# Kernel tuning notes

Measured on AMD Instinct MI355X. Metric: run time of the kernel, lower is better.

Reference implementation:

```python
import jax, jax.numpy as jnp
import numpy as np

N_WORDS, MAX_LEN = 16384, 16
VOCAB, EMB, HID = 128, 64, 256


def setup_inputs() -> dict:
    key = jax.random.key(0)
    ks = jax.random.split(key, 11)
    s = 1.0 / np.sqrt(HID)  # torch LSTMCell default init scale
    u = lambda k, shape: jax.random.uniform(k, shape, jnp.float32, -s, s)
    return {
        "char_ids": jax.random.randint(ks[0], (N_WORDS, MAX_LEN), 0, VOCAB, dtype=jnp.int32),
        "lengths": jax.random.randint(ks[1], (N_WORDS,), 1, MAX_LEN + 1, dtype=jnp.int32),
        "emb": jax.random.normal(ks[2], (VOCAB, EMB), jnp.float32),
        "W_ih_f": u(ks[3], (4 * HID, EMB)),
        "W_hh_f": u(ks[4], (4 * HID, HID)),
        "b_ih_f": u(ks[5], (4 * HID,)),
        "b_hh_f": u(ks[6], (4 * HID,)),
        "W_ih_b": u(ks[7], (4 * HID, EMB)),
        "W_hh_b": u(ks[8], (4 * HID, HID)),
        "b_ih_b": u(ks[9], (4 * HID,)),
        "b_hh_b": u(ks[10], (4 * HID,)),
    }


def _run_lstm(xs, mask, W_ih, W_hh, b):
    # xs: [T, N, E]; mask: [T, N]; returns final masked hidden state [N, H]
    n = xs.shape[1]
    h0 = jnp.zeros((n, W_hh.shape[1]), xs.dtype)

    def step(carry, inp):
        h, c = carry
        x, m = inp
        gates = x @ W_ih.T + h @ W_hh.T + b  # [N, 4H], torch gate order i,f,g,o
        i, f, g, o = jnp.split(gates, 4, axis=-1)
        c2 = jax.nn.sigmoid(f) * c + jax.nn.sigmoid(i) * jnp.tanh(g)
        h2 = jax.nn.sigmoid(o) * jnp.tanh(c2)
        m = m[:, None]
        return (jnp.where(m, h2, h), jnp.where(m, c2, c)), None

    (h, _), _ = jax.lax.scan(step, (h0, h0), (xs, mask))
    return h


def reference(char_ids, lengths, emb, W_ih_f, W_hh_f, b_ih_f, b_hh_f,
              W_ih_b, W_hh_b, b_ih_b, b_hh_b):
    x = emb[char_ids]                                   # [N, T, E]
    t = jnp.arange(MAX_LEN)
    mask = t[None, :] < lengths[:, None]                # [N, T] valid chars
    xs = x.transpose(1, 0, 2)                           # [T, N, E]
    ms = mask.T                                         # [T, N]
    h_f = _run_lstm(xs, ms, W_ih_f, W_hh_f, b_ih_f + b_hh_f)
    # per-word reversed sequence: chars processed from last to first
    ridx = jnp.clip(lengths[:, None] - 1 - t[None, :], 0)  # [N, T]
    xr = jnp.take_along_axis(x, ridx[:, :, None], axis=1)  # [N, T, E]
    h_b = _run_lstm(xr.transpose(1, 0, 2), ms, W_ih_b, W_hh_b, b_ih_b + b_hh_b)
    return jnp.concatenate([h_f, h_b], axis=-1)         # [N, 2H]
```

## Files before the change

### kernel.cpp

```cpp
#include <hip/hip_runtime.h>

#define N_WORDS 16384
#define MAXL    16
#define VOCABSZ 128
#define EMBD    64
#define HID     256
#define GATES   1024
#define KTOT    320
#define AROW    328
#define M_TILE  64
#define NT      256

typedef __attribute__((ext_vector_type(8))) short bf16x8;
typedef __attribute__((ext_vector_type(4))) float f32x4;
typedef __attribute__((ext_vector_type(4))) int   i32x4;

#define OFF_WSW   0ul
#define OFF_EMB   1310720ul
#define OFF_BIAS  1327104ul
#define OFF_SORT  1335296ul

__device__ inline short tobf(float f) {
  unsigned u = __float_as_uint(f);
  unsigned r = (u + 0x7fffu + ((u >> 16) & 1u)) >> 16;
  return (short)r;
}
__device__ inline float aexp2(float x) { float r; asm("v_exp_f32 %0, %1" : "=v"(r) : "v"(x)); return r; }
__device__ inline float arcp(float x)  { float r; asm("v_rcp_f32 %0, %1" : "=v"(r) : "v"(x)); return r; }
__device__ inline float fsig(float x)   { return arcp(1.0f + aexp2(x * -1.4426950408889634f)); }
__device__ inline float ftanhf(float x) { return 1.0f - 2.0f * arcp(1.0f + aexp2(x * 2.8853900817779268f)); }

__global__ void prep_all(const float* __restrict__ Wihf, const float* __restrict__ Whhf,
                         const float* __restrict__ Wihb, const float* __restrict__ Whhb,
                         const float* __restrict__ emb,
                         const float* __restrict__ bihf, const float* __restrict__ bhhf,
                         const float* __restrict__ bihb, const float* __restrict__ bhhb,
                         const int* __restrict__ lengths,
                         short* __restrict__ wsw, short* __restrict__ embw,
                         float* __restrict__ biasg, int* __restrict__ sorted) {
  __shared__ int hist[16], base[16], cnt[16];
  int blk = blockIdx.x;
  if (blk < 320) {
    int id = blk * 256 + threadIdx.x;
    int d    = id / 40960;
    int r    = id % 40960;
    int R    = r / 640;
    int r2   = r % 640;
    int kk   = r2 / 64;
    int lane = r2 % 64;
    int m    = lane & 15;
    int unit = R * 4 + (m >> 2);
    int ty   = m & 3;
    int g    = ty * 256 + unit;
    int kb   = kk * 32 + (lane >> 4) * 8;
    const float* Wih = d ? Wihb : Wihf;
    const float* Whh = d ? Whhb : Whhf;
    bf16x8 v;
#pragma unroll
    for (int j = 0; j < 8; ++j) {
      int k = kb + j;
      float f = (k < HID) ? Whh[g * HID + k] : Wih[g * EMBD + (k - HID)];
      v[j] = tobf(f);
    }
    ((bf16x8*)wsw)[id] = v;
  } else if (blk < 360) {
    int id = (blk - 320) * 256 + threadIdx.x;
    if (id < VOCABSZ * EMBD) {
      embw[id] = tobf(emb[id]);
    } else {
      int r = id - VOCABSZ * EMBD;
      if (r < 2048) {
        int d = r >> 10, n = r & 1023;
        int g = (n & 3) * 256 + (n >> 2);
        biasg[r] = d ? (bihb[g] + bhhb[g]) : (bihf[g] + bhhf[g]);
      }
    }
  } else {
    int tid = threadIdx.x;
    if (tid < 16) { hist[tid] = 0; cnt[tid] = 0; }
    __syncthreads();
    for (int i = tid; i < N_WORDS; i += 256)
      atomicAdd(&hist[lengths[i] - 1], 1);
    __syncthreads();
    if (tid == 0) {
      int s = 0;
      for (int b = 0; b < 16; ++b) { base[b] = s; s += hist[b]; }
    }
    __syncthreads();
    for (int i = tid; i < N_WORDS; i += 256) {
      int b = lengths[i] - 1;
      int p = base[b] + atomicAdd(&cnt[b], 1);
      sorted[p] = i;
    }
  }
}

__global__ __launch_bounds__(512, 1) void lstm_main(
    const int* __restrict__ char_ids, const int* __restrict__ lengths,
    const short* __restrict__ wsw, const short* __restrict__ embw,
    const float* __restrict__ biasg, const int* __restrict__ sorted,
    float* __restrict__ out) {
  __shared__ __align__(16) short A[M_TILE * AROW];
  __shared__ __align__(16) int   charl[M_TILE * 16];
  __shared__ __align__(16) float biasl[GATES];
  __shared__ __align__(16) f32x4 c4[8 * 8 * 64];
  __shared__ int lenl[M_TILE];
  __shared__ int swl[M_TILE];

  const int tid  = threadIdx.x;
  const int lane = tid & 63;
  const int wv   = tid >> 6;
  const int quad = lane >> 4;
  const int colc = lane & 15;
  const int pb   = blockIdx.x;
  const int dir  = pb & 1;
  const int qb   = pb >> 1;
  const int tile = (qb & 1) ? (255 - (qb >> 1)) : (qb >> 1);

  if (tid < M_TILE) {
    int sw = sorted[tile * M_TILE + tid];
    swl[tid]  = sw;
    lenl[tid] = lengths[sw];
  }
  if (tid < 256) ((f32x4*)biasl)[tid] = ((const f32x4*)(biasg + dir * GATES))[tid];
  for (int i = tid; i < M_TILE * AROW / 2; i += 512) ((int*)A)[i] = 0;
  for (int i = tid; i < 8 * 8 * 64; i += 512) c4[i] = (f32x4){0.f, 0.f, 0.f, 0.f};
  __syncthreads();

  if (tid < 256) {
    int w = tid >> 2, ch = tid & 3;
    ((i32x4*)charl)[tid] = ((const i32x4*)(char_ids + swl[w] * 16))[ch];
  }
  int Lmax = lenl[lane];
  for (int o = 32; o; o >>= 1) { int v = __shfl_xor(Lmax, o, 64); Lmax = Lmax > v ? Lmax : v; }
  __syncthreads();

  auto gather_x = [&](int tt) {
    int wl = wv * 8 + (lane >> 3);
    int part = lane & 7;
    int lw = lenl[wl];
    int pos = (dir == 0) ? tt : (lw - 1 - tt);
    pos = pos < 0 ? 0 : (pos > 15 ? 15 : pos);
    int cid = charl[wl * 16 + pos];
    bf16x8 e = *(const bf16x8*)(embw + cid * EMBD + part * 8);
    *(bf16x8*)(A + wl * AROW + HID + part * 8) = e;
  };
  gather_x(0);

  int lenw[4], hadrb[4], oadr[4];
#pragma unroll
  for (int ct = 0; ct < 4; ++ct) {
    int wl = ct * 16 + colc;
    lenw[ct]  = lenl[wl];
    hadrb[ct] = wl * AROW + 32 * wv + quad;
    oadr[ct]  = swl[wl] * 512 + dir * 256 + 32 * wv + quad;
  }
  const short* wp = wsw + ((size_t)dir * 64 + wv * 8) * 10 * 64 * 8 + lane * 8;
  f32x4* cptr = c4 + wv * (8 * 64) + lane;

  __syncthreads();

  bf16x8 wA[10], wB[10];
#pragma unroll
  for (int kk = 0; kk < 10; ++kk) wA[kk] = *(const bf16x8*)(wp + kk * 512);

#pragma unroll 1
  for (int t = 0; t < Lmax; ++t) {
    bf16x8 hx[4][10];
#pragma unroll
    for (int ct = 0; ct < 4; ++ct)
#pragma unroll
      for (int kk = 0; kk < 10; ++kk)
        hx[ct][kk] = *(const bf16x8*)(A + (ct * 16 + colc) * AROW + kk * 32 + quad * 8);

    __syncthreads();

    auto wtile = [&](int rt, bf16x8(&wc)[10], bf16x8(&wn)[10], int pre) {
#pragma unroll
      for (int kk = 0; kk < 10; ++kk) wn[kk] = *(const bf16x8*)(wp + (pre * 10 + kk) * 512);
      f32x4 co4 = cptr[rt * 64];
      f32x4 bias4 = *(const f32x4*)(biasl + 128 * wv + 16 * rt + 4 * quad);
      f32x4 acc[4];
#pragma unroll
      for (int ct = 0; ct < 4; ++ct) acc[ct] = bias4;
#pragma unroll
      for (int kk = 0; kk < 10; ++kk)
#pragma unroll
        for (int ct = 0; ct < 4; ++ct)
          acc[ct] = __builtin_amdgcn_mfma_f32_16x16x32_bf16(wc[kk], hx[ct][kk], acc[ct], 0, 0, 0);

      f32x4 cnew;
#pragma unroll
      for (int ct = 0; ct < 4; ++ct) {
        float ig = fsig(acc[ct][0]);
        float fg = fsig(acc[ct][1]);
        float gg = ftanhf(acc[ct][2]);
        float og = fsig(acc[ct][3]);
        float co_v = co4[ct];
        float c2 = fg * co_v + ig * gg;
        float h2 = og * ftanhf(c2);
        bool act = t < lenw[ct];
        cnew[ct] = act ? c2 : co_v;
        if (act) A[hadrb[ct] + 4 * rt] = tobf(h2);
        if (t == lenw[ct] - 1) out[oadr[ct] + 4 * rt] = h2;
      }
      cptr[rt * 64] = cnew;
    };

#pragma unroll 1
    for (int rt2 = 0; rt2 < 8; rt2 += 2) {
      wtile(rt2,     wA, wB, rt2 + 1);
      wtile(rt2 + 1, wB, wA, (rt2 + 2) & 7);
    }

    gather_x(t + 1);
    __syncthreads();
  }
}

extern "C" void kernel_launch(void* const* d_in, const int* in_sizes, int n_in,
                              void* d_out, int out_size, void* d_ws, size_t ws_size,
                              hipStream_t stream) {
  const int*   char_ids = (const int*)d_in[0];
  const int*   lengths  = (const int*)d_in[1];
  const float* emb      = (const float*)d_in[2];
  const float* Wihf     = (const float*)d_in[3];
  const float* Whhf     = (const float*)d_in[4];
  const float* bihf     = (const float*)d_in[5];
  const float* bhhf     = (const float*)d_in[6];
  const float* Wihb     = (const float*)d_in[7];
  const float* Whhb     = (const float*)d_in[8];
  const float* bihb     = (const float*)d_in[9];
  const float* bhhb     = (const float*)d_in[10];

  char* ws = (char*)d_ws;
  short* wsw   = (short*)(ws + OFF_WSW);
  short* embw  = (short*)(ws + OFF_EMB);
  float* biasg = (float*)(ws + OFF_BIAS);
  int*   sortd = (int*)(ws + OFF_SORT);

  prep_all<<<361, 256, 0, stream>>>(Wihf, Whhf, Wihb, Whhb, emb,
                                    bihf, bhhf, bihb, bhhb, lengths,
                                    wsw, embw, biasg, sortd);
  lstm_main<<<512, 512, 0, stream>>>(char_ids, lengths, wsw, embw, biasg, sortd,
                                     (float*)d_out);
}
```

Baseline: 405.2 us.

## Double-buffer LSTM hidden-state tile to drop one barrier per timestep

Splits the shared A tile into two ping-pong buffers so each step reads h from one buffer and writes the new h into the other. This removes the mid-step __syncthreads, leaving a single raw s_barrier per step. The embedding gather is issued before the last two gate tiles so its latency overlaps MFMA work. The length masking on c and h is dropped, so words keep updating after their last character; this relies on outputs being written at t==len-1 and the sorted-by-length tiles. Costs an extra 42KB of LDS.

```diff
diff --git a/kernel.cpp b/kernel.cpp
--- a/kernel.cpp
+++ b/kernel.cpp
@@ -100,7 +100,8 @@
     const short* __restrict__ wsw, const short* __restrict__ embw,
     const float* __restrict__ biasg, const int* __restrict__ sorted,
     float* __restrict__ out) {
-  __shared__ __align__(16) short A[M_TILE * AROW];
+  __shared__ __align__(16) short A0[M_TILE * AROW];
+  __shared__ __align__(16) short A1[M_TILE * AROW];
   __shared__ __align__(16) int   charl[M_TILE * 16];
   __shared__ __align__(16) float biasl[GATES];
   __shared__ __align__(16) f32x4 c4[8 * 8 * 64];
@@ -123,7 +124,7 @@
     lenl[tid] = lengths[sw];
   }
   if (tid < 256) ((f32x4*)biasl)[tid] = ((const f32x4*)(biasg + dir * GATES))[tid];
-  for (int i = tid; i < M_TILE * AROW / 2; i += 512) ((int*)A)[i] = 0;
+  for (int i = tid; i < M_TILE * AROW / 2; i += 512) ((int*)A0)[i] = 0;
   for (int i = tid; i < 8 * 8 * 64; i += 512) c4[i] = (f32x4){0.f, 0.f, 0.f, 0.f};
   __syncthreads();
 
@@ -135,17 +136,19 @@
   for (int o = 32; o; o >>= 1) { int v = __shfl_xor(Lmax, o, 64); Lmax = Lmax > v ? Lmax : v; }
   __syncthreads();
 
-  auto gather_x = [&](int tt) {
-    int wl = wv * 8 + (lane >> 3);
-    int part = lane & 7;
-    int lw = lenl[wl];
+  const int xwl   = wv * 8 + (lane >> 3);
+  const int xpart = lane & 7;
+  auto x_load = [&](int tt) -> bf16x8 {
+    int lw = lenl[xwl];
     int pos = (dir == 0) ? tt : (lw - 1 - tt);
     pos = pos < 0 ? 0 : (pos > 15 ? 15 : pos);
-    int cid = charl[wl * 16 + pos];
-    bf16x8 e = *(const bf16x8*)(embw + cid * EMBD + part * 8);
-    *(bf16x8*)(A + wl * AROW + HID + part * 8) = e;
+    int cid = charl[xwl * 16 + pos];
+    return *(const bf16x8*)(embw + cid * EMBD + xpart * 8);
   };
-  gather_x(0);
+  auto x_store = [&](short* An, bf16x8 e) {
+    *(bf16x8*)(An + xwl * AROW + HID + xpart * 8) = e;
+  };
+  x_store(A0, x_load(0));
 
   int lenw[4], hadrb[4], oadr[4];
 #pragma unroll
@@ -164,6 +167,9 @@
 #pragma unroll
   for (int kk = 0; kk < 10; ++kk) wA[kk] = *(const bf16x8*)(wp + kk * 512);
 
+  short* Ac = A0;
+  short* An = A1;
+
 #pragma unroll 1
   for (int t = 0; t < Lmax; ++t) {
     bf16x8 hx[4][10];
@@ -171,9 +177,7 @@
     for (int ct = 0; ct < 4; ++ct)
 #pragma unroll
       for (int kk = 0; kk < 10; ++kk)
-        hx[ct][kk] = *(const bf16x8*)(A + (ct * 16 + colc) * AROW + kk * 32 + quad * 8);
-
-    __syncthreads();
+        hx[ct][kk] = *(const bf16x8*)(Ac + (ct * 16 + colc) * AROW + kk * 32 + quad * 8);
 
     auto wtile = [&](int rt, bf16x8(&wc)[10], bf16x8(&wn)[10], int pre) {
 #pragma unroll
@@ -196,25 +200,27 @@
         float fg = fsig(acc[ct][1]);
         float gg = ftanhf(acc[ct][2]);
         float og = fsig(acc[ct][3]);
-        float co_v = co4[ct];
-        float c2 = fg * co_v + ig * gg;
+        float c2 = fg * co4[ct] + ig * gg;
         float h2 = og * ftanhf(c2);
-        bool act = t < lenw[ct];
-        cnew[ct] = act ? c2 : co_v;
-        if (act) A[hadrb[ct] + 4 * rt] = tobf(h2);
+        cnew[ct] = c2;
+        An[hadrb[ct] + 4 * rt] = tobf(h2);
         if (t == lenw[ct] - 1) out[oadr[ct] + 4 * rt] = h2;
       }
       cptr[rt * 64] = cnew;
     };
 
 #pragma unroll 1
-    for (int rt2 = 0; rt2 < 8; rt2 += 2) {
+    for (int rt2 = 0; rt2 < 6; rt2 += 2) {
       wtile(rt2,     wA, wB, rt2 + 1);
-      wtile(rt2 + 1, wB, wA, (rt2 + 2) & 7);
-    }
-
-    gather_x(t + 1);
-    __syncthreads();
+      wtile(rt2 + 1, wB, wA, rt2 + 2);
+    }
+    bf16x8 e = x_load(t + 1);
+    wtile(6, wA, wB, 7);
+    wtile(7, wB, wA, 0);
+    x_store(An, e);
+
+    asm volatile("s_waitcnt lgkmcnt(0)\n\ts_barrier" ::: "memory");
+    short* tmp = Ac; Ac = An; An = tmp;
   }
 }
 
```

Result: slower. 573.9 us (+41.6%).

## Halve word tile to 32, run two 256-thread blocks per CU, split MFMA chains

Applied to the files above, without the earlier changes.

Each LSTM block now handles 32 length-sorted words with 4 waves, and each wave covers 16 gate row-tiles instead of 8. There are 1024 blocks at two per CU, so one block's barrier-bound recurrence can overlap another's. Each MFMA accumulation is split into two independent chains for more instruction-level parallelism. Masking of h/c writes after a word ends is dropped, since outputs are captured at the last valid step. In exchange, the weight stream is re-read by twice as many blocks, which raises L2/global weight traffic per word.

```diff
diff --git a/kernel.cpp b/kernel.cpp
--- a/kernel.cpp
+++ b/kernel.cpp
@@ -8,11 +8,12 @@
 #define GATES   1024
 #define KTOT    320
 #define AROW    328
-#define M_TILE  64
-#define NT      256
+#define M_TILE  32
+#define NT      512
 
 typedef __attribute__((ext_vector_type(8))) short bf16x8;
 typedef __attribute__((ext_vector_type(4))) float f32x4;
+typedef __attribute__((ext_vector_type(2))) float f32x2;
 typedef __attribute__((ext_vector_type(4))) int   i32x4;
 
 #define OFF_WSW   0ul
@@ -95,7 +96,7 @@
   }
 }
 
-__global__ __launch_bounds__(512, 1) void lstm_main(
+__global__ __launch_bounds__(256, 2) void lstm_main(
     const int* __restrict__ char_ids, const int* __restrict__ lengths,
     const short* __restrict__ wsw, const short* __restrict__ embw,
     const float* __restrict__ biasg, const int* __restrict__ sorted,
@@ -103,7 +104,7 @@
   __shared__ __align__(16) short A[M_TILE * AROW];
   __shared__ __align__(16) int   charl[M_TILE * 16];
   __shared__ __align__(16) float biasl[GATES];
-  __shared__ __align__(16) f32x4 c4[8 * 8 * 64];
+  __shared__ __align__(8)  f32x2 c4[4 * 16 * 64];
   __shared__ int lenl[M_TILE];
   __shared__ int swl[M_TILE];
 
@@ -115,23 +116,23 @@
   const int pb   = blockIdx.x;
   const int dir  = pb & 1;
   const int qb   = pb >> 1;
-  const int tile = (qb & 1) ? (255 - (qb >> 1)) : (qb >> 1);
+  const int tile = (qb & 1) ? (511 - (qb >> 1)) : (qb >> 1);
 
   if (tid < M_TILE) {
     int sw = sorted[tile * M_TILE + tid];
     swl[tid]  = sw;
     lenl[tid] = lengths[sw];
   }
-  if (tid < 256) ((f32x4*)biasl)[tid] = ((const f32x4*)(biasg + dir * GATES))[tid];
-  for (int i = tid; i < M_TILE * AROW / 2; i += 512) ((int*)A)[i] = 0;
-  for (int i = tid; i < 8 * 8 * 64; i += 512) c4[i] = (f32x4){0.f, 0.f, 0.f, 0.f};
+  ((f32x4*)biasl)[tid] = ((const f32x4*)(biasg + dir * GATES))[tid];
+  for (int i = tid; i < M_TILE * AROW / 2; i += 256) ((int*)A)[i] = 0;
+  for (int i = tid; i < 4 * 16 * 64; i += 256) c4[i] = (f32x2){0.f, 0.f};
   __syncthreads();
 
-  if (tid < 256) {
+  if (tid < 128) {
     int w = tid >> 2, ch = tid & 3;
     ((i32x4*)charl)[tid] = ((const i32x4*)(char_ids + swl[w] * 16))[ch];
   }
-  int Lmax = lenl[lane];
+  int Lmax = lenl[lane & 31];
   for (int o = 32; o; o >>= 1) { int v = __shfl_xor(Lmax, o, 64); Lmax = Lmax > v ? Lmax : v; }
   __syncthreads();
 
@@ -147,16 +148,16 @@
   };
   gather_x(0);
 
-  int lenw[4], hadrb[4], oadr[4];
-#pragma unroll
-  for (int ct = 0; ct < 4; ++ct) {
+  int lenw[2], hadrb[2], oadr[2];
+#pragma unroll
+  for (int ct = 0; ct < 2; ++ct) {
     int wl = ct * 16 + colc;
     lenw[ct]  = lenl[wl];
-    hadrb[ct] = wl * AROW + 32 * wv + quad;
-    oadr[ct]  = swl[wl] * 512 + dir * 256 + 32 * wv + quad;
-  }
-  const short* wp = wsw + ((size_t)dir * 64 + wv * 8) * 10 * 64 * 8 + lane * 8;
-  f32x4* cptr = c4 + wv * (8 * 64) + lane;
+    hadrb[ct] = wl * AROW + 64 * wv + quad;
+    oadr[ct]  = swl[wl] * 512 + dir * 256 + 64 * wv + quad;
+  }
+  const short* wp = wsw + ((size_t)dir * 64 + wv * 16) * 10 * 64 * 8 + lane * 8;
+  f32x2* cptr = c4 + wv * (16 * 64) + lane;
 
   __syncthreads();
 
@@ -166,9 +167,9 @@
 
 #pragma unroll 1
   for (int t = 0; t < Lmax; ++t) {
-    bf16x8 hx[4][10];
-#pragma unroll
-    for (int ct = 0; ct < 4; ++ct)
+    bf16x8 hx[2][10];
+#pragma unroll
+    for (int ct = 0; ct < 2; ++ct)
 #pragma unroll
       for (int kk = 0; kk < 10; ++kk)
         hx[ct][kk] = *(const bf16x8*)(A + (ct * 16 + colc) * AROW + kk * 32 + quad * 8);
@@ -178,39 +179,40 @@
     auto wtile = [&](int rt, bf16x8(&wc)[10], bf16x8(&wn)[10], int pre) {
 #pragma unroll
       for (int kk = 0; kk < 10; ++kk) wn[kk] = *(const bf16x8*)(wp + (pre * 10 + kk) * 512);
-      f32x4 co4 = cptr[rt * 64];
-      f32x4 bias4 = *(const f32x4*)(biasl + 128 * wv + 16 * rt + 4 * quad);
-      f32x4 acc[4];
-#pragma unroll
-      for (int ct = 0; ct < 4; ++ct) acc[ct] = bias4;
-#pragma unroll
-      for (int kk = 0; kk < 10; ++kk)
-#pragma unroll
-        for (int ct = 0; ct < 4; ++ct)
-          acc[ct] = __builtin_amdgcn_mfma_f32_16x16x32_bf16(wc[kk], hx[ct][kk], acc[ct], 0, 0, 0);
-
-      f32x4 cnew;
-#pragma unroll
-      for (int ct = 0; ct < 4; ++ct) {
-        float ig = fsig(acc[ct][0]);
-        float fg = fsig(acc[ct][1]);
-        float gg = ftanhf(acc[ct][2]);
-        float og = fsig(acc[ct][3]);
-        float co_v = co4[ct];
-        float c2 = fg * co_v + ig * gg;
+      f32x2 co2 = cptr[rt * 64];
+      f32x4 bias4 = *(const f32x4*)(biasl + 256 * wv + 16 * rt + 4 * quad);
+      f32x4 aL[2], aH[2];
+#pragma unroll
+      for (int ct = 0; ct < 2; ++ct) { aL[ct] = bias4; aH[ct] = (f32x4){0.f,0.f,0.f,0.f}; }
+#pragma unroll
+      for (int kk = 0; kk < 5; ++kk)
+#pragma unroll
+        for (int ct = 0; ct < 2; ++ct) {
+          aL[ct] = __builtin_amdgcn_mfma_f32_16x16x32_bf16(wc[kk],     hx[ct][kk],     aL[ct], 0, 0, 0);
+          aH[ct] = __builtin_amdgcn_mfma_f32_16x16x32_bf16(wc[kk + 5], hx[ct][kk + 5], aH[ct], 0, 0, 0);
+        }
+
+      f32x2 cnew;
+#pragma unroll
+      for (int ct = 0; ct < 2; ++ct) {
+        f32x4 acc = aL[ct] + aH[ct];
+        float ig = fsig(acc[0]);
+        float fg = fsig(acc[1]);
+        float gg = ftanhf(acc[2]);
+        float og = fsig(acc[3]);
+        float c2 = fg * co2[ct] + ig * gg;
         float h2 = og * ftanhf(c2);
-        bool act = t < lenw[ct];
-        cnew[ct] = act ? c2 : co_v;
-        if (act) A[hadrb[ct] + 4 * rt] = tobf(h2);
+        cnew[ct] = c2;
+        A[hadrb[ct] + 4 * rt] = tobf(h2);
         if (t == lenw[ct] - 1) out[oadr[ct] + 4 * rt] = h2;
       }
       cptr[rt * 64] = cnew;
     };
 
 #pragma unroll 1
-    for (int rt2 = 0; rt2 < 8; rt2 += 2) {
+    for (int rt2 = 0; rt2 < 16; rt2 += 2) {
       wtile(rt2,     wA, wB, rt2 + 1);
-      wtile(rt2 + 1, wB, wA, (rt2 + 2) & 7);
+      wtile(rt2 + 1, wB, wA, (rt2 + 2) & 15);
     }
 
     gather_x(t + 1);
@@ -242,6 +244,6 @@
   prep_all<<<361, 256, 0, stream>>>(Wihf, Whhf, Wihb, Whhb, emb,
                                     bihf, bhhf, bihb, bhhb, lengths,
                                     wsw, embw, biasg, sortd);
-  lstm_main<<<512, 512, 0, stream>>>(char_ids, lengths, wsw, embw, biasg, sortd,
-                                     (float*)d_out);
-}
+  lstm_main<<<1024, 256, 0, stream>>>(char_ids, lengths, wsw, embw, biasg, sortd,
+                                      (float*)d_out);
+}
```

Result: slower. 438.4 us (+8.2%).
